# Kernel tuning notes

Hardware: AMD Instinct MI355X
Metric: run time of the kernel (lower is better)

## Reference

```python
import jax, jax.numpy as jnp
import numpy as np

DIM = 512
HEADS = 8
DIM_HEAD = 64
SLICE = 32
INNER = HEADS * DIM_HEAD  # 512


def setup_inputs() -> dict:
    key = jax.random.key(0)
    ks = jax.random.split(key, 8)
    B, N = 8, 8192
    s = 0.02
    return {
        "x": jax.random.normal(ks[0], (B, N, DIM), dtype=jnp.float32),
        "W_in": jax.random.normal(ks[1], (DIM, INNER), dtype=jnp.float32) * s,
        "b_in": jnp.zeros((INNER,), dtype=jnp.float32),
        "Wq": jax.random.normal(ks[2], (DIM_HEAD, SLICE), dtype=jnp.float32) * s,
        "Wk": jax.random.normal(ks[3], (DIM_HEAD, SLICE), dtype=jnp.float32) * s,
        "Wv": jax.random.normal(ks[4], (DIM_HEAD, DIM_HEAD), dtype=jnp.float32) * s,
        "W_out": jax.random.normal(ks[5], (INNER, DIM), dtype=jnp.float32) * s,
        "b_out": jnp.zeros((DIM,), dtype=jnp.float32),
    }


def reference(x, W_in, b_in, Wq, Wk, Wv, W_out, b_out):
    B, N, C = x.shape
    # input projection -> [B, H, N, Dh]
    x_mid = (x @ W_in + b_in).reshape(B, N, HEADS, DIM_HEAD).transpose(0, 2, 1, 3)
    q = x_mid @ Wq            # [B,H,N,S]
    k = x_mid @ Wk            # [B,H,N,S]
    v = x_mid @ Wv            # [B,H,N,Dh]
    q = jax.nn.softmax(q, axis=-1)   # over slice dim
    k = jax.nn.softmax(k, axis=-2)   # over sequence dim
    kv = jnp.einsum('bhns,bhnc->bhsc', k, v)   # [B,H,S,Dh]
    qkv = jnp.einsum('bhns,bhsc->bhnc', q, kv)  # [B,H,N,Dh]
    qkv = qkv.transpose(0, 2, 1, 3).reshape(B, N, INNER)  # b n (h d)
    return qkv @ W_out + b_out
```

## Files before the change

### kernel.cpp

```cpp
#include <hip/hip_runtime.h>
#include <cstdint>
#include <cstddef>

typedef __bf16 bf16_t;
typedef __bf16 bf16x8 __attribute__((ext_vector_type(8)));
typedef __bf16 bf16x4 __attribute__((ext_vector_type(4)));
typedef float  f32x4  __attribute__((ext_vector_type(4)));

#define HEADS    8
#define DIM_HEAD 64
#define SLICE    32
#define DIMC     512
#define NCOL     1024
#define BATCH    8
#define NSEQ     8192
#define NTOK     65536

__device__ __forceinline__ void gl2lds16(const bf16_t* g, bf16_t* l) {
  __builtin_amdgcn_global_load_lds(
      (const __attribute__((address_space(1))) uint32_t*)g,
      (__attribute__((address_space(3))) uint32_t*)l, 16, 0, 0);
}

__global__ __launch_bounds__(256) void xcast_kernel(const float* __restrict__ x,
                                                    bf16_t* __restrict__ xb) {
  const size_t i = ((size_t)blockIdx.x * 256 + threadIdx.x) * 8;
  const float4 a = *reinterpret_cast<const float4*>(x + i);
  const float4 b = *reinterpret_cast<const float4*>(x + i + 4);
  bf16x8 w;
  w[0] = (bf16_t)a.x; w[1] = (bf16_t)a.y; w[2] = (bf16_t)a.z; w[3] = (bf16_t)a.w;
  w[4] = (bf16_t)b.x; w[5] = (bf16_t)b.y; w[6] = (bf16_t)b.z; w[7] = (bf16_t)b.w;
  *reinterpret_cast<bf16x8*>(xb + i) = w;
}

__global__ __launch_bounds__(256) void wprep_kernel(
    const float* __restrict__ W_in, const float* __restrict__ b_in,
    const float* __restrict__ Wq,   const float* __restrict__ Wk,
    const float* __restrict__ Wv,
    bf16_t* __restrict__ WcT, float* __restrict__ bias_c) {
  __shared__ float sW[8192];
  for (int t = threadIdx.x; t < 2048; t += 256) { sW[t] = Wq[t]; sW[2048 + t] = Wk[t]; }
  for (int t = threadIdx.x; t < 4096; t += 256) sW[4096 + t] = Wv[t];
  __syncthreads();

  const int T  = blockIdx.x * 256 + threadIdx.x;
  const int NT = gridDim.x * 256;
  for (int idx = T; idx < NCOL * DIMC; idx += NT) {
    const int col = idx >> 9, cin = idx & 511;
    const int h = col >> 7, r = col & 127;
    int base, ldw, j;
    if (r < 32)      { j = r;      base = 0;    ldw = 32; }
    else if (r < 64) { j = r - 32; base = 2048; ldw = 32; }
    else             { j = r - 64; base = 4096; ldw = 64; }
    const float4* vp = reinterpret_cast<const float4*>(W_in + (size_t)cin * DIMC + h * DIM_HEAD);
    float acc = 0.f;
    #pragma unroll
    for (int d4 = 0; d4 < 16; ++d4) {
      const float4 v = vp[d4];
      acc += v.x * sW[base + (4*d4+0)*ldw + j];
      acc += v.y * sW[base + (4*d4+1)*ldw + j];
      acc += v.z * sW[base + (4*d4+2)*ldw + j];
      acc += v.w * sW[base + (4*d4+3)*ldw + j];
    }
    WcT[(size_t)col * DIMC + cin] = (bf16_t)acc;
  }
  if (T < NCOL) {
    const int col = T;
    const int h = col >> 7, r = col & 127;
    int base, ldw, j;
    if (r < 32)      { j = r;      base = 0;    ldw = 32; }
    else if (r < 64) { j = r - 32; base = 2048; ldw = 32; }
    else             { j = r - 64; base = 4096; ldw = 64; }
    const float* vec = b_in + h * DIM_HEAD;
    float acc = 0.f;
    #pragma unroll 8
    for (int d = 0; d < DIM_HEAD; ++d) acc += vec[d] * sW[base + d * ldw + j];
    bias_c[col] = acc;
  }
}

template<int EPI>
__global__ __launch_bounds__(256) void gemm_kernel(
    const bf16_t* __restrict__ A, const bf16_t* __restrict__ Bt,
    void* __restrict__ Cv, const float* __restrict__ bias,
    int K, int lda, int ldc,
    size_t strideA, size_t strideB, size_t strideC,
    float* __restrict__ kvp_g, float* __restrict__ denp_g)
{
  __shared__ bf16_t As[128 * 64];
  __shared__ bf16_t Bs[128 * 64];
  const int tid = threadIdx.x;
  const int p = blockIdx.y * gridDim.x + blockIdx.x;
  int mblk, nblk;
  if (EPI == 1) { mblk = (p & 7) + ((p >> 6) << 3); nblk = (p >> 3) & 7; }
  else          { mblk = (p & 7) + ((p >> 5) << 3); nblk = (p >> 3) & 3; }
  const int m0 = mblk * 128;
  const int n0 = nblk * 128;
  const int bz = blockIdx.z;
  const int wave = tid >> 6, lane = tid & 63;
  const int cg   = lane & 15, qd = lane >> 4;
  const int wm   = (wave & 1) * 64, wn = (wave >> 1) * 64;
  const int srw    = lane >> 3;
  const int gchunk = (lane & 7) ^ srw;
  const int chb    = cg & 7;

  const bf16_t* Ab = A  + strideA * bz;
  const bf16_t* Bb = Bt + strideB * bz;

  f32x4 acc[4][4];
  #pragma unroll
  for (int i = 0; i < 4; ++i)
    #pragma unroll
    for (int j = 0; j < 4; ++j) acc[i][j] = (f32x4){0.f, 0.f, 0.f, 0.f};

  for (int k0 = 0; k0 < K; k0 += 64) {
    __syncthreads();
    #pragma unroll
    for (int i = 0; i < 4; ++i) {
      const int c = wave * 4 + i;
      const int row = c * 8 + srw;
      gl2lds16(Ab + (size_t)(m0 + row) * lda + k0 + gchunk * 8, As + c * 512 + lane * 8);
    }
    #pragma unroll
    for (int i = 0; i < 4; ++i) {
      const int c = wave * 4 + i;
      const int row = c * 8 + srw;
      gl2lds16(Bb + (size_t)(n0 + row) * K + k0 + gchunk * 8, Bs + c * 512 + lane * 8);
    }
    __syncthreads();
    #pragma unroll
    for (int ks = 0; ks < 64; ks += 32) {
      const int k4 = ks >> 3;
      bf16x8 af[4], bfr[4];
      #pragma unroll
      for (int i = 0; i < 4; ++i) {
        const int ch = (qd + k4) ^ chb;
        af[i] = *reinterpret_cast<const bf16x8*>(As + (wm + 16*i + cg) * 64 + ch * 8);
      }
      #pragma unroll
      for (int j = 0; j < 4; ++j) {
        const int ch = (qd + k4) ^ chb;
        bfr[j] = *reinterpret_cast<const bf16x8*>(Bs + (wn + 16*j + cg) * 64 + ch * 8);
      }
      #pragma unroll
      for (int i = 0; i < 4; ++i)
        #pragma unroll
        for (int j = 0; j < 4; ++j)
          acc[i][j] = __builtin_amdgcn_mfma_f32_16x16x32_bf16(af[i], bfr[j], acc[i][j], 0, 0, 0);
    }
  }

  if (EPI == 1) {
    const int h   = nblk;
    const int bat = mblk >> 6;
    const int mb  = mblk & 63;
    const int bh  = bat * HEADS + h;
    __syncthreads();
    bf16_t* ekT   = As;
    bf16_t* vT    = Bs;
    float*  den_s = (float*)(void*)(As + 4096);

    if (wave < 2) {
      {
        const float b0 = bias[n0 + cg];
        const float b1 = bias[n0 + 16 + cg];
        #pragma unroll
        for (int i = 0; i < 4; ++i) {
          #pragma unroll
          for (int rr = 0; rr < 4; ++rr) {
            float v0 = acc[i][0][rr] + b0;
            float v1 = acc[i][1][rr] + b1;
            float mx = fmaxf(v0, v1);
            #pragma unroll
            for (int d = 1; d < 16; d <<= 1) mx = fmaxf(mx, __shfl_xor(mx, d, 64));
            const float e0 = __expf(v0 - mx), e1 = __expf(v1 - mx);
            float ssum = e0 + e1;
            #pragma unroll
            for (int d = 1; d < 16; d <<= 1) ssum += __shfl_xor(ssum, d, 64);
            const float rs = 1.f / ssum;
            const int row = m0 + wm + 16 * i + qd * 4 + rr;
            bf16_t* crow = (bf16_t*)Cv + (size_t)row * ldc + h * SLICE;
            crow[cg]      = (bf16_t)(e0 * rs);
            crow[16 + cg] = (bf16_t)(e1 * rs);
          }
        }
      }
      #pragma unroll
      for (int j = 2; j < 4; ++j) {
        const int s = 16 * (j - 2) + cg;
        const float bb = bias[n0 + 16 * j + cg];
        float dsum = 0.f;
        #pragma unroll
        for (int i = 0; i < 4; ++i) {
          #pragma unroll
          for (int rr = 0; rr < 4; ++rr) {
            const float e = __expf(acc[i][j][rr] + bb);
            dsum += e;
            const int n = wm + 16 * i + qd * 4 + rr;
            *(bf16_t*)((char*)ekT + (((s << 8) + 2 * n) ^ ((s & 7) << 4))) = (bf16_t)e;
          }
        }
        dsum += __shfl_xor(dsum, 16, 64);
        dsum += __shfl_xor(dsum, 32, 64);
        if (qd == 0) den_s[wave * 32 + s] = dsum;
      }
    } else {
      #pragma unroll
      for (int j = 0; j < 4; ++j) {
        const int c = 16 * j + cg;
        const float bb = bias[n0 + 64 + c];
        #pragma unroll
        for (int i = 0; i < 4; ++i) {
          #pragma unroll
          for (int rr = 0; rr < 4; ++rr) {
            const float vv = acc[i][j][rr] + bb;
            const int n = wm + 16 * i + qd * 4 + rr;
            *(bf16_t*)((char*)vT + (((c << 8) + 2 * n) ^ ((c & 7) << 4))) = (bf16_t)vv;
          }
        }
      }
    }
    __syncthreads();
    if (tid < SLICE)
      denp_g[((size_t)bh * 64 + mb) * SLICE + tid] = den_s[tid] + den_s[32 + tid];

    const int st = wave & 1;
    const int sA = st * 16 + cg;
    float* kvp = kvp_g + ((size_t)bh * 64 + mb) * (SLICE * DIM_HEAD);
    #pragma unroll
    for (int ci = 0; ci < 2; ++ci) {
      const int ct = (wave >> 1) * 2 + ci;
      const int cB = ct * 16 + cg;
      f32x4 kacc = (f32x4){0.f, 0.f, 0.f, 0.f};
      #pragma unroll
      for (int ks = 0; ks < 4; ++ks) {
        bf16x8 afr = *(const bf16x8*)((const char*)ekT +
                       (((sA << 8) + ks * 64 + qd * 16) ^ ((sA & 7) << 4)));
        bf16x8 bfr2 = *(const bf16x8*)((const char*)vT +
                       (((cB << 8) + ks * 64 + qd * 16) ^ ((cB & 7) << 4)));
        kacc = __builtin_amdgcn_mfma_f32_16x16x32_bf16(afr, bfr2, kacc, 0, 0, 0);
      }
      #pragma unroll
      for (int r = 0; r < 4; ++r)
        kvp[(st * 16 + qd * 4 + r) * DIM_HEAD + ct * 16 + cg] = kacc[r];
    }
  } else {
    #pragma unroll
    for (int j = 0; j < 4; ++j) {
      const int col = n0 + wn + 16 * j + cg;
      const float bv = bias[col];
      #pragma unroll
      for (int i = 0; i < 4; ++i) {
        #pragma unroll
        for (int rr = 0; rr < 4; ++rr) {
          const int row = m0 + wm + 16 * i + qd * 4 + rr;
          ((float*)Cv + strideC * bz)[(size_t)row * ldc + col] = acc[i][j][rr] + bv;
        }
      }
    }
  }
}

__global__ __launch_bounds__(512) void mprep_kernel(const float* __restrict__ kv_part,
                                                    const float* __restrict__ den_part,
                                                    const float* __restrict__ W_out,
                                                    bf16_t* __restrict__ Mt) {
  const int bh = blockIdx.x, bat = bh >> 3, h = bh & 7;
  const int tid = threadIdx.x;
  __shared__ float kvn[SLICE][DIM_HEAD];
  __shared__ float dsh[SLICE];
  __shared__ float wbuf[8][DIMC];
  const float* np = kv_part + (size_t)bh * 64 * (SLICE * DIM_HEAD);
  if (tid < SLICE) {
    const float* dp = den_part + (size_t)bh * 64 * SLICE;
    float d = 0.f;
    for (int mb = 0; mb < 64; ++mb) d += dp[mb * SLICE + tid];
    dsh[tid] = d;
  }
  float a0 = 0.f, a1 = 0.f, a2 = 0.f, a3 = 0.f;
  for (int mb = 0; mb < 64; ++mb) {
    const float* qp = np + (size_t)mb * (SLICE * DIM_HEAD);
    a0 += qp[tid]; a1 += qp[tid + 512]; a2 += qp[tid + 1024]; a3 += qp[tid + 1536];
  }
  __syncthreads();
  kvn[tid >> 6][tid & 63]            = a0 / dsh[tid >> 6];
  kvn[(tid + 512) >> 6][tid & 63]    = a1 / dsh[(tid + 512) >> 6];
  kvn[(tid + 1024) >> 6][tid & 63]   = a2 / dsh[(tid + 1024) >> 6];
  kvn[(tid + 1536) >> 6][tid & 63]   = a3 / dsh[(tid + 1536) >> 6];

  float accs[SLICE];
  #pragma unroll
  for (int s = 0; s < SLICE; ++s) accs[s] = 0.f;
  for (int cb = 0; cb < DIM_HEAD; cb += 8) {
    __syncthreads();
    for (int t = tid; t < 8 * DIMC; t += 512)
      wbuf[t >> 9][t & 511] = W_out[(size_t)(h * DIM_HEAD + cb + (t >> 9)) * DIMC + (t & 511)];
    __syncthreads();
    #pragma unroll
    for (int cc = 0; cc < 8; ++cc) {
      const float wv = wbuf[cc][tid];
      #pragma unroll
      for (int s = 0; s < SLICE; ++s) accs[s] += kvn[s][cb + cc] * wv;
    }
  }
  bf16_t* dst = Mt + (size_t)bat * (DIMC * 256) + (size_t)tid * 256 + h * SLICE;
  #pragma unroll
  for (int s = 0; s < SLICE; ++s) dst[s] = (bf16_t)accs[s];
}

extern "C" void kernel_launch(void* const* d_in, const int* in_sizes, int n_in,
                              void* d_out, int out_size, void* d_ws, size_t ws_size,
                              hipStream_t stream) {
  const float* x     = (const float*)d_in[0];
  const float* W_in  = (const float*)d_in[1];
  const float* b_in  = (const float*)d_in[2];
  const float* Wq    = (const float*)d_in[3];
  const float* Wk    = (const float*)d_in[4];
  const float* Wv    = (const float*)d_in[5];
  const float* W_out = (const float*)d_in[6];
  const float* b_out = (const float*)d_in[7];

  uint8_t* ws = (uint8_t*)d_ws;
  bf16_t* qprime   = (bf16_t*)(ws);
  bf16_t* WcT      = (bf16_t*)(ws + 33554432ull);
  float*  bias_c   = (float*) (ws + 34603008ull);
  float*  kv_part  = (float*) (ws + 34607104ull);
  float*  den_part = (float*) (ws + 68161536ull);
  bf16_t* Mt       = (bf16_t*)(ws + 68685824ull);
  bf16_t* xb = (bf16_t*)d_out;

  xcast_kernel<<<dim3(NTOK * DIMC / 8 / 256), dim3(256), 0, stream>>>(x, xb);
  wprep_kernel<<<dim3(256), dim3(256), 0, stream>>>(W_in, b_in, Wq, Wk, Wv, WcT, bias_c);

  gemm_kernel<1><<<dim3(8, 512, 1), dim3(256), 0, stream>>>(
      xb, WcT, (void*)qprime, bias_c,
      512 , 512 , 256 , (size_t)0, (size_t)0, (size_t)0,
      kv_part, den_part);

  mprep_kernel<<<dim3(BATCH * HEADS), dim3(512), 0, stream>>>(kv_part, den_part, W_out, Mt);

  gemm_kernel<0><<<dim3(4, 64, BATCH), dim3(256), 0, stream>>>(
      qprime, Mt, d_out, b_out,
      256 , 256 , DIMC ,
      (size_t)NSEQ * 256, (size_t)DIMC * 256, (size_t)NSEQ * DIMC,
      nullptr, nullptr);
}
```

Before: 451.2 us.

## Use 256x256 tiles with double-buffered LDS pipeline and split kv reduction

Result: slower. 502.6 us (+11.4%).

```diff
diff --git a/kernel.cpp b/kernel.cpp
--- a/kernel.cpp
+++ b/kernel.cpp
@@ -4,14 +4,12 @@
 
 typedef __bf16 bf16_t;
 typedef __bf16 bf16x8 __attribute__((ext_vector_type(8)));
-typedef __bf16 bf16x4 __attribute__((ext_vector_type(4)));
 typedef float  f32x4  __attribute__((ext_vector_type(4)));
 
 #define HEADS    8
 #define DIM_HEAD 64
 #define SLICE    32
 #define DIMC     512
-#define NCOL     1024
 #define BATCH    8
 #define NSEQ     8192
 #define NTOK     65536
@@ -45,7 +43,7 @@
 
   const int T  = blockIdx.x * 256 + threadIdx.x;
   const int NT = gridDim.x * 256;
-  for (int idx = T; idx < NCOL * DIMC; idx += NT) {
+  for (int idx = T; idx < 1024 * DIMC; idx += NT) {
     const int col = idx >> 9, cin = idx & 511;
     const int h = col >> 7, r = col & 127;
     int base, ldw, j;
@@ -64,7 +62,7 @@
     }
     WcT[(size_t)col * DIMC + cin] = (bf16_t)acc;
   }
-  if (T < NCOL) {
+  if (T < 1024) {
     const int col = T;
     const int h = col >> 7, r = col & 127;
     int base, ldw, j;
@@ -80,169 +78,180 @@
 }
 
 template<int EPI>
-__global__ __launch_bounds__(256) void gemm_kernel(
+__global__ __launch_bounds__(512, 2) void gemm_kernel(
     const bf16_t* __restrict__ A, const bf16_t* __restrict__ Bt,
     void* __restrict__ Cv, const float* __restrict__ bias,
     int K, int lda, int ldc,
     size_t strideA, size_t strideB, size_t strideC,
     float* __restrict__ kvp_g, float* __restrict__ denp_g)
 {
-  __shared__ bf16_t As[128 * 64];
-  __shared__ bf16_t Bs[128 * 64];
+  __shared__ char smem[65536];
   const int tid = threadIdx.x;
   const int p = blockIdx.y * gridDim.x + blockIdx.x;
   int mblk, nblk;
-  if (EPI == 1) { mblk = (p & 7) + ((p >> 6) << 3); nblk = (p >> 3) & 7; }
-  else          { mblk = (p & 7) + ((p >> 5) << 3); nblk = (p >> 3) & 3; }
-  const int m0 = mblk * 128;
-  const int n0 = nblk * 128;
+  if (EPI == 1) { mblk = (p & 7) + ((p >> 5) << 3); nblk = (p >> 3) & 3; }
+  else          { mblk = (p & 7) + ((p >> 4) << 3); nblk = (p >> 3) & 1; }
+  const int m0 = mblk * 256, n0 = nblk * 256;
   const int bz = blockIdx.z;
   const int wave = tid >> 6, lane = tid & 63;
-  const int cg   = lane & 15, qd = lane >> 4;
-  const int wm   = (wave & 1) * 64, wn = (wave >> 1) * 64;
-  const int srw    = lane >> 3;
-  const int gchunk = (lane & 7) ^ srw;
-  const int chb    = cg & 7;
+  const int cg = lane & 15, qd = lane >> 4;
+  const int wmi = wave >> 2;
+  const int wm = wmi * 128, wn = (wave & 3) * 64;
+  const int srow   = tid >> 2;
+  const int gchunk = (tid & 3) ^ ((tid >> 4) & 3);
 
   const bf16_t* Ab = A  + strideA * bz;
   const bf16_t* Bb = Bt + strideB * bz;
 
-  f32x4 acc[4][4];
+  auto stageA = [&](int ko, int buf) {
+    #pragma unroll
+    for (int p2 = 0; p2 < 2; ++p2)
+      gl2lds16(Ab + (size_t)(m0 + p2 * 128 + srow) * lda + ko + gchunk * 8,
+               (bf16_t*)(smem + buf * 16384 + p2 * 8192 + tid * 16));
+  };
+  auto stageB = [&](int ko, int buf) {
+    #pragma unroll
+    for (int p2 = 0; p2 < 2; ++p2)
+      gl2lds16(Bb + (size_t)(n0 + p2 * 128 + srow) * K + ko + gchunk * 8,
+               (bf16_t*)(smem + 32768 + buf * 16384 + p2 * 8192 + tid * 16));
+  };
+  auto ldA = [&](int buf, int r) -> bf16x8 {
+    return *(const bf16x8*)(smem + buf * 16384 + r * 64 + ((qd ^ ((r >> 2) & 3)) << 4));
+  };
+  auto ldB = [&](int buf, int r) -> bf16x8 {
+    return *(const bf16x8*)(smem + 32768 + buf * 16384 + r * 64 + ((qd ^ ((r >> 2) & 3)) << 4));
+  };
+
+  f32x4 acc[8][4];
   #pragma unroll
-  for (int i = 0; i < 4; ++i)
+  for (int i = 0; i < 8; ++i)
     #pragma unroll
     for (int j = 0; j < 4; ++j) acc[i][j] = (f32x4){0.f, 0.f, 0.f, 0.f};
 
-  for (int k0 = 0; k0 < K; k0 += 64) {
+  stageA(0, 0);
+  stageB(0, 0);
+
+  const int T = K >> 5;
+  int cur = 0;
+  for (int t = 0; t < T; ++t) {
+    const int nxt = cur ^ 1;
+    const int kn = (t + 1) << 5;
+    const bool pf = (t + 1 < T);
+
+    if (pf) { stageA(kn, nxt); asm volatile("s_waitcnt vmcnt(2)" ::: "memory"); }
+    else    { asm volatile("s_waitcnt vmcnt(0)" ::: "memory"); }
+    __builtin_amdgcn_s_barrier();
+
+    bf16x8 bF[4], aF[4];
+    #pragma unroll
+    for (int j = 0; j < 4; ++j) bF[j] = ldB(cur, wn + 16 * j + cg);
+    #pragma unroll
+    for (int i = 0; i < 4; ++i) aF[i] = ldA(cur, wm + 16 * i + cg);
+    __builtin_amdgcn_s_setprio(1);
+    #pragma unroll
+    for (int i = 0; i < 4; ++i)
+      #pragma unroll
+      for (int j = 0; j < 4; ++j)
+        acc[i][j] = __builtin_amdgcn_mfma_f32_16x16x32_bf16(aF[i], bF[j], acc[i][j], 0, 0, 0);
+    __builtin_amdgcn_s_setprio(0);
+
+    if (pf) stageB(kn, nxt);
+    bf16x8 aG[4];
+    #pragma unroll
+    for (int i = 0; i < 4; ++i) aG[i] = ldA(cur, wm + 64 + 16 * i + cg);
+    __builtin_amdgcn_s_setprio(1);
+    #pragma unroll
+    for (int i = 0; i < 4; ++i)
+      #pragma unroll
+      for (int j = 0; j < 4; ++j)
+        acc[i + 4][j] = __builtin_amdgcn_mfma_f32_16x16x32_bf16(aG[i], bF[j], acc[i + 4][j], 0, 0, 0);
+    __builtin_amdgcn_s_setprio(0);
+    __builtin_amdgcn_s_barrier();
+    cur = nxt;
+  }
+
+  if (EPI == 1) {
     __syncthreads();
-    #pragma unroll
-    for (int i = 0; i < 4; ++i) {
-      const int c = wave * 4 + i;
-      const int row = c * 8 + srw;
-      gl2lds16(Ab + (size_t)(m0 + row) * lda + k0 + gchunk * 8, As + c * 512 + lane * 8);
-    }
-    #pragma unroll
-    for (int i = 0; i < 4; ++i) {
-      const int c = wave * 4 + i;
-      const int row = c * 8 + srw;
-      gl2lds16(Bb + (size_t)(n0 + row) * K + k0 + gchunk * 8, Bs + c * 512 + lane * 8);
-    }
-    __syncthreads();
-    #pragma unroll
-    for (int ks = 0; ks < 64; ks += 32) {
-      const int k4 = ks >> 3;
-      bf16x8 af[4], bfr[4];
-      #pragma unroll
-      for (int i = 0; i < 4; ++i) {
-        const int ch = (qd + k4) ^ chb;
-        af[i] = *reinterpret_cast<const bf16x8*>(As + (wm + 16*i + cg) * 64 + ch * 8);
-      }
-      #pragma unroll
-      for (int j = 0; j < 4; ++j) {
-        const int ch = (qd + k4) ^ chb;
-        bfr[j] = *reinterpret_cast<const bf16x8*>(Bs + (wn + 16*j + cg) * 64 + ch * 8);
-      }
-      #pragma unroll
-      for (int i = 0; i < 4; ++i)
+    const int role = wave & 3;
+    const int bat = mblk >> 5, mb = mblk & 31;
+    char*  ekT   = smem;
+    char*  vT    = smem + 32768;
+    float* den_s = (float*)(smem + 16384);
+
+    for (int h = 0; h < 2; ++h) {
+      if (role == 2 * h) {
+        const float bq0 = bias[n0 + h * 128 + cg];
+        const float bq1 = bias[n0 + h * 128 + 16 + cg];
         #pragma unroll
-        for (int j = 0; j < 4; ++j)
-          acc[i][j] = __builtin_amdgcn_mfma_f32_16x16x32_bf16(af[i], bfr[j], acc[i][j], 0, 0, 0);
-    }
-  }
-
-  if (EPI == 1) {
-    const int h   = nblk;
-    const int bat = mblk >> 6;
-    const int mb  = mblk & 63;
-    const int bh  = bat * HEADS + h;
-    __syncthreads();
-    bf16_t* ekT   = As;
-    bf16_t* vT    = Bs;
-    float*  den_s = (float*)(void*)(As + 4096);
-
-    if (wave < 2) {
-      {
-        const float b0 = bias[n0 + cg];
-        const float b1 = bias[n0 + 16 + cg];
-        #pragma unroll
-        for (int i = 0; i < 4; ++i) {
+        for (int i = 0; i < 8; ++i) {
           #pragma unroll
           for (int rr = 0; rr < 4; ++rr) {
-            float v0 = acc[i][0][rr] + b0;
-            float v1 = acc[i][1][rr] + b1;
-            float mx = fmaxf(v0, v1);
+            const float e0 = __expf(acc[i][0][rr] + bq0);
+            const float e1 = __expf(acc[i][1][rr] + bq1);
+            float s = e0 + e1;
             #pragma unroll
-            for (int d = 1; d < 16; d <<= 1) mx = fmaxf(mx, __shfl_xor(mx, d, 64));
-            const float e0 = __expf(v0 - mx), e1 = __expf(v1 - mx);
-            float ssum = e0 + e1;
-            #pragma unroll
-            for (int d = 1; d < 16; d <<= 1) ssum += __shfl_xor(ssum, d, 64);
-            const float rs = 1.f / ssum;
+            for (int d = 1; d < 16; d <<= 1) s += __shfl_xor(s, d, 64);
+            const float rs = 1.f / s;
             const int row = m0 + wm + 16 * i + qd * 4 + rr;
-            bf16_t* crow = (bf16_t*)Cv + (size_t)row * ldc + h * SLICE;
+            bf16_t* crow = (bf16_t*)Cv + (size_t)row * ldc + (nblk * 2 + h) * SLICE;
             crow[cg]      = (bf16_t)(e0 * rs);
             crow[16 + cg] = (bf16_t)(e1 * rs);
           }
         }
-      }
-      #pragma unroll
-      for (int j = 2; j < 4; ++j) {
-        const int s = 16 * (j - 2) + cg;
-        const float bb = bias[n0 + 16 * j + cg];
-        float dsum = 0.f;
         #pragma unroll
-        for (int i = 0; i < 4; ++i) {
+        for (int j = 2; j < 4; ++j) {
+          const int s_i = 16 * (j - 2) + cg;
+          const float bk = bias[n0 + h * 128 + 32 + 16 * (j - 2) + cg];
+          float dsum = 0.f;
           #pragma unroll
-          for (int rr = 0; rr < 4; ++rr) {
-            const float e = __expf(acc[i][j][rr] + bb);
-            dsum += e;
-            const int n = wm + 16 * i + qd * 4 + rr;
-            *(bf16_t*)((char*)ekT + (((s << 8) + 2 * n) ^ ((s & 7) << 4))) = (bf16_t)e;
+          for (int i = 0; i < 8; ++i) {
+            #pragma unroll
+            for (int rr = 0; rr < 4; ++rr) {
+              const float e = __expf(acc[i][j][rr] + bk);
+              dsum += e;
+              const int n = wm + 16 * i + qd * 4 + rr;
+              *(bf16_t*)(ekT + (s_i << 9) + ((2 * n) ^ ((s_i & 7) << 4))) = (bf16_t)e;
+            }
           }
+          dsum += __shfl_xor(dsum, 16, 64);
+          dsum += __shfl_xor(dsum, 32, 64);
+          if (qd == 0) den_s[wmi * 32 + s_i] = dsum;
         }
-        dsum += __shfl_xor(dsum, 16, 64);
-        dsum += __shfl_xor(dsum, 32, 64);
-        if (qd == 0) den_s[wave * 32 + s] = dsum;
-      }
-    } else {
-      #pragma unroll
-      for (int j = 0; j < 4; ++j) {
-        const int c = 16 * j + cg;
-        const float bb = bias[n0 + 64 + c];
+      } else if (role == 2 * h + 1) {
         #pragma unroll
-        for (int i = 0; i < 4; ++i) {
+        for (int j = 0; j < 4; ++j) {
+          const int c = 16 * j + cg;
+          const float bv = bias[n0 + h * 128 + 64 + c];
           #pragma unroll
-          for (int rr = 0; rr < 4; ++rr) {
-            const float vv = acc[i][j][rr] + bb;
-            const int n = wm + 16 * i + qd * 4 + rr;
-            *(bf16_t*)((char*)vT + (((c << 8) + 2 * n) ^ ((c & 7) << 4))) = (bf16_t)vv;
+          for (int i = 0; i < 8; ++i) {
+            #pragma unroll
+            for (int rr = 0; rr < 4; ++rr) {
+              const float vv = acc[i][j][rr] + bv;
+              const int n = wm + 16 * i + qd * 4 + rr;
+              *(bf16_t*)(vT + (c << 9) + ((2 * n) ^ ((c & 7) << 4))) = (bf16_t)vv;
+            }
           }
         }
       }
-    }
-    __syncthreads();
-    if (tid < SLICE)
-      denp_g[((size_t)bh * 64 + mb) * SLICE + tid] = den_s[tid] + den_s[32 + tid];
-
-    const int st = wave & 1;
-    const int sA = st * 16 + cg;
-    float* kvp = kvp_g + ((size_t)bh * 64 + mb) * (SLICE * DIM_HEAD);
-    #pragma unroll
-    for (int ci = 0; ci < 2; ++ci) {
-      const int ct = (wave >> 1) * 2 + ci;
+      __syncthreads();
+      const int bh = bat * HEADS + nblk * 2 + h;
+      if (tid < SLICE)
+        denp_g[((size_t)bh * 32 + mb) * SLICE + tid] = den_s[tid] + den_s[32 + tid];
+      const int st = wave & 1, ct = wave >> 1;
+      const int sA = st * 16 + cg;
       const int cB = ct * 16 + cg;
       f32x4 kacc = (f32x4){0.f, 0.f, 0.f, 0.f};
       #pragma unroll
-      for (int ks = 0; ks < 4; ++ks) {
-        bf16x8 afr = *(const bf16x8*)((const char*)ekT +
-                       (((sA << 8) + ks * 64 + qd * 16) ^ ((sA & 7) << 4)));
-        bf16x8 bfr2 = *(const bf16x8*)((const char*)vT +
-                       (((cB << 8) + ks * 64 + qd * 16) ^ ((cB & 7) << 4)));
-        kacc = __builtin_amdgcn_mfma_f32_16x16x32_bf16(afr, bfr2, kacc, 0, 0, 0);
+      for (int kk = 0; kk < 8; ++kk) {
+        const bf16x8 afr = *(const bf16x8*)(ekT + (sA << 9) + ((kk * 64 + qd * 16) ^ ((sA & 7) << 4)));
+        const bf16x8 bfr = *(const bf16x8*)(vT  + (cB << 9) + ((kk * 64 + qd * 16) ^ ((cB & 7) << 4)));
+        kacc = __builtin_amdgcn_mfma_f32_16x16x32_bf16(afr, bfr, kacc, 0, 0, 0);
       }
+      float* kvp = kvp_g + ((size_t)bh * 32 + mb) * 2048;
       #pragma unroll
       for (int r = 0; r < 4; ++r)
-        kvp[(st * 16 + qd * 4 + r) * DIM_HEAD + ct * 16 + cg] = kacc[r];
+        kvp[(st * 16 + qd * 4 + r) * 64 + cB] = kacc[r];
+      __syncthreads();
     }
   } else {
     #pragma unroll
@@ -250,7 +259,7 @@
       const int col = n0 + wn + 16 * j + cg;
       const float bv = bias[col];
       #pragma unroll
-      for (int i = 0; i < 4; ++i) {
+      for (int i = 0; i < 8; ++i) {
         #pragma unroll
         for (int rr = 0; rr < 4; ++rr) {
           const int row = m0 + wm + 16 * i + qd * 4 + rr;
@@ -261,32 +270,37 @@
   }
 }
 
-__global__ __launch_bounds__(512) void mprep_kernel(const float* __restrict__ kv_part,
-                                                    const float* __restrict__ den_part,
+__global__ __launch_bounds__(256) void kvreduce_kernel(const float* __restrict__ kv_part,
+                                                       const float* __restrict__ den_part,
+                                                       float* __restrict__ kv_red,
+                                                       float* __restrict__ den_red) {
+  const int ch = blockIdx.x, bh = blockIdx.y;
+  const int tid = threadIdx.x;
+  const float* src = kv_part + (size_t)bh * 32 * 2048 + ch * 256 + tid;
+  float s = 0.f;
+  #pragma unroll
+  for (int mb = 0; mb < 32; ++mb) s += src[(size_t)mb * 2048];
+  kv_red[(size_t)bh * 2048 + ch * 256 + tid] = s;
+  if (ch == 0 && tid < 32) {
+    const float* dsrc = den_part + (size_t)bh * 32 * 32 + tid;
+    float d = 0.f;
+    #pragma unroll
+    for (int mb = 0; mb < 32; ++mb) d += dsrc[mb * 32];
+    den_red[bh * 32 + tid] = d;
+  }
+}
+
+__global__ __launch_bounds__(512) void mprep_kernel(const float* __restrict__ kv_red,
+                                                    const float* __restrict__ den_red,
                                                     const float* __restrict__ W_out,
                                                     bf16_t* __restrict__ Mt) {
   const int bh = blockIdx.x, bat = bh >> 3, h = bh & 7;
   const int tid = threadIdx.x;
   __shared__ float kvn[SLICE][DIM_HEAD];
-  __shared__ float dsh[SLICE];
   __shared__ float wbuf[8][DIMC];
-  const float* np = kv_part + (size_t)bh * 64 * (SLICE * DIM_HEAD);
-  if (tid < SLICE) {
-    const float* dp = den_part + (size_t)bh * 64 * SLICE;
-    float d = 0.f;
-    for (int mb = 0; mb < 64; ++mb) d += dp[mb * SLICE + tid];
-    dsh[tid] = d;
-  }
-  float a0 = 0.f, a1 = 0.f, a2 = 0.f, a3 = 0.f;
-  for (int mb = 0; mb < 64; ++mb) {
-    const float* qp = np + (size_t)mb * (SLICE * DIM_HEAD);
-    a0 += qp[tid]; a1 += qp[tid + 512]; a2 += qp[tid + 1024]; a3 += qp[tid + 1536];
-  }
-  __syncthreads();
-  kvn[tid >> 6][tid & 63]            = a0 / dsh[tid >> 6];
-  kvn[(tid + 512) >> 6][tid & 63]    = a1 / dsh[(tid + 512) >> 6];
-  kvn[(tid + 1024) >> 6][tid & 63]   = a2 / dsh[(tid + 1024) >> 6];
-  kvn[(tid + 1536) >> 6][tid & 63]   = a3 / dsh[(tid + 1536) >> 6];
+  const float* src = kv_red + (size_t)bh * 2048;
+  const float* dp  = den_red + bh * 32;
+  for (int t = tid; t < 2048; t += 512) kvn[t >> 6][t & 63] = src[t] / dp[t >> 6];
 
   float accs[SLICE];
   #pragma unroll
@@ -325,21 +339,24 @@
   bf16_t* WcT      = (bf16_t*)(ws + 33554432ull);
   float*  bias_c   = (float*) (ws + 34603008ull);
   float*  kv_part  = (float*) (ws + 34607104ull);
-  float*  den_part = (float*) (ws + 68161536ull);
-  bf16_t* Mt       = (bf16_t*)(ws + 68685824ull);
+  float*  den_part = (float*) (ws + 51384320ull);
+  float*  kv_red   = (float*) (ws + 51646464ull);
+  float*  den_red  = (float*) (ws + 52170752ull);
+  bf16_t* Mt       = (bf16_t*)(ws + 52178944ull);
   bf16_t* xb = (bf16_t*)d_out;
 
   xcast_kernel<<<dim3(NTOK * DIMC / 8 / 256), dim3(256), 0, stream>>>(x, xb);
   wprep_kernel<<<dim3(256), dim3(256), 0, stream>>>(W_in, b_in, Wq, Wk, Wv, WcT, bias_c);
 
-  gemm_kernel<1><<<dim3(8, 512, 1), dim3(256), 0, stream>>>(
+  gemm_kernel<1><<<dim3(8, 128, 1), dim3(512), 0, stream>>>(
       xb, WcT, (void*)qprime, bias_c,
       512 , 512 , 256 , (size_t)0, (size_t)0, (size_t)0,
       kv_part, den_part);
 
-  mprep_kernel<<<dim3(BATCH * HEADS), dim3(512), 0, stream>>>(kv_part, den_part, W_out, Mt);
-
-  gemm_kernel<0><<<dim3(4, 64, BATCH), dim3(256), 0, stream>>>(
+  kvreduce_kernel<<<dim3(8, 64), dim3(256), 0, stream>>>(kv_part, den_part, kv_red, den_red);
+  mprep_kernel<<<dim3(BATCH * HEADS), dim3(512), 0, stream>>>(kv_red, den_red, W_out, Mt);
+
+  gemm_kernel<0><<<dim3(8, 8, BATCH), dim3(512), 0, stream>>>(
       qprime, Mt, d_out, b_out,
       256 , 256 , DIMC ,
       (size_t)NSEQ * 256, (size_t)DIMC * 256, (size_t)NSEQ * DIMC,
```

## Fuse fp32-to-bf16 cast into first GEMM and parallelize kv reduction

Applied to the files above, without the earlier changes.

Result: slower. 525.4 us (+16.4%).

```diff
diff --git a/kernel.cpp b/kernel.cpp
--- a/kernel.cpp
+++ b/kernel.cpp
@@ -4,14 +4,12 @@
 
 typedef __bf16 bf16_t;
 typedef __bf16 bf16x8 __attribute__((ext_vector_type(8)));
-typedef __bf16 bf16x4 __attribute__((ext_vector_type(4)));
 typedef float  f32x4  __attribute__((ext_vector_type(4)));
 
 #define HEADS    8
 #define DIM_HEAD 64
 #define SLICE    32
 #define DIMC     512
-#define NCOL     1024
 #define BATCH    8
 #define NSEQ     8192
 #define NTOK     65536
@@ -20,17 +18,6 @@
   __builtin_amdgcn_global_load_lds(
       (const __attribute__((address_space(1))) uint32_t*)g,
       (__attribute__((address_space(3))) uint32_t*)l, 16, 0, 0);
-}
-
-__global__ __launch_bounds__(256) void xcast_kernel(const float* __restrict__ x,
-                                                    bf16_t* __restrict__ xb) {
-  const size_t i = ((size_t)blockIdx.x * 256 + threadIdx.x) * 8;
-  const float4 a = *reinterpret_cast<const float4*>(x + i);
-  const float4 b = *reinterpret_cast<const float4*>(x + i + 4);
-  bf16x8 w;
-  w[0] = (bf16_t)a.x; w[1] = (bf16_t)a.y; w[2] = (bf16_t)a.z; w[3] = (bf16_t)a.w;
-  w[4] = (bf16_t)b.x; w[5] = (bf16_t)b.y; w[6] = (bf16_t)b.z; w[7] = (bf16_t)b.w;
-  *reinterpret_cast<bf16x8*>(xb + i) = w;
 }
 
 __global__ __launch_bounds__(256) void wprep_kernel(
@@ -45,7 +32,7 @@
 
   const int T  = blockIdx.x * 256 + threadIdx.x;
   const int NT = gridDim.x * 256;
-  for (int idx = T; idx < NCOL * DIMC; idx += NT) {
+  for (int idx = T; idx < 1024 * DIMC; idx += NT) {
     const int col = idx >> 9, cin = idx & 511;
     const int h = col >> 7, r = col & 127;
     int base, ldw, j;
@@ -64,7 +51,7 @@
     }
     WcT[(size_t)col * DIMC + cin] = (bf16_t)acc;
   }
-  if (T < NCOL) {
+  if (T < 1024) {
     const int col = T;
     const int h = col >> 7, r = col & 127;
     int base, ldw, j;
@@ -79,33 +66,28 @@
   }
 }
 
-template<int EPI>
-__global__ __launch_bounds__(256) void gemm_kernel(
-    const bf16_t* __restrict__ A, const bf16_t* __restrict__ Bt,
-    void* __restrict__ Cv, const float* __restrict__ bias,
-    int K, int lda, int ldc,
-    size_t strideA, size_t strideB, size_t strideC,
+__global__ __launch_bounds__(256) void gemm1_kernel(
+    const float* __restrict__ X, const bf16_t* __restrict__ Bt,
+    bf16_t* __restrict__ qprime, const float* __restrict__ bias,
     float* __restrict__ kvp_g, float* __restrict__ denp_g)
 {
   __shared__ bf16_t As[128 * 64];
   __shared__ bf16_t Bs[128 * 64];
   const int tid = threadIdx.x;
   const int p = blockIdx.y * gridDim.x + blockIdx.x;
-  int mblk, nblk;
-  if (EPI == 1) { mblk = (p & 7) + ((p >> 6) << 3); nblk = (p >> 3) & 7; }
-  else          { mblk = (p & 7) + ((p >> 5) << 3); nblk = (p >> 3) & 3; }
-  const int m0 = mblk * 128;
-  const int n0 = nblk * 128;
-  const int bz = blockIdx.z;
+  const int mblk = (p & 7) + ((p >> 6) << 3);
+  const int nblk = (p >> 3) & 7;
+  const int m0 = mblk * 128, n0 = nblk * 128;
   const int wave = tid >> 6, lane = tid & 63;
-  const int cg   = lane & 15, qd = lane >> 4;
-  const int wm   = (wave & 1) * 64, wn = (wave >> 1) * 64;
-  const int srw    = lane >> 3;
+  const int cg = lane & 15, qd = lane >> 4;
+  const int wm = (wave & 1) * 64, wn = (wave >> 1) * 64;
+  const int srw = lane >> 3;
   const int gchunk = (lane & 7) ^ srw;
-  const int chb    = cg & 7;
-
-  const bf16_t* Ab = A  + strideA * bz;
-  const bf16_t* Bb = Bt + strideB * bz;
+  const int chb = cg & 7;
+
+  const int arow = tid >> 1;
+  const int akh  = (tid & 1) * 32;
+  const float* xrow = X + (size_t)(m0 + arow) * DIMC + akh;
 
   f32x4 acc[4][4];
   #pragma unroll
@@ -113,21 +95,39 @@
     #pragma unroll
     for (int j = 0; j < 4; ++j) acc[i][j] = (f32x4){0.f, 0.f, 0.f, 0.f};
 
-  for (int k0 = 0; k0 < K; k0 += 64) {
+  float4 xr[8];
+  #pragma unroll
+  for (int l = 0; l < 8; ++l) xr[l] = *reinterpret_cast<const float4*>(xrow + l * 4);
+
+  for (int k0 = 0; k0 < DIMC; k0 += 64) {
     __syncthreads();
+    #pragma unroll
+    for (int c = 0; c < 4; ++c) {
+      const float4 u = xr[2 * c], v = xr[2 * c + 1];
+      bf16x8 w;
+      w[0] = (bf16_t)u.x; w[1] = (bf16_t)u.y; w[2] = (bf16_t)u.z; w[3] = (bf16_t)u.w;
+      w[4] = (bf16_t)v.x; w[5] = (bf16_t)v.y; w[6] = (bf16_t)v.z; w[7] = (bf16_t)v.w;
+      const int g = (akh >> 3) + c;
+      *reinterpret_cast<bf16x8*>(As + arow * 64 + ((g ^ (arow & 7)) << 3)) = w;
+    }
     #pragma unroll
     for (int i = 0; i < 4; ++i) {
       const int c = wave * 4 + i;
       const int row = c * 8 + srw;
-      gl2lds16(Ab + (size_t)(m0 + row) * lda + k0 + gchunk * 8, As + c * 512 + lane * 8);
-    }
-    #pragma unroll
-    for (int i = 0; i < 4; ++i) {
-      const int c = wave * 4 + i;
-      const int row = c * 8 + srw;
-      gl2lds16(Bb + (size_t)(n0 + row) * K + k0 + gchunk * 8, Bs + c * 512 + lane * 8);
-    }
-    __syncthreads();
+      gl2lds16(Bt + (size_t)(n0 + row) * DIMC + k0 + gchunk * 8, Bs + c * 512 + lane * 8);
+    }
+    __builtin_amdgcn_sched_barrier(0);
+    if (k0 + 64 < DIMC) {
+      #pragma unroll
+      for (int l = 0; l < 8; ++l)
+        xr[l] = *reinterpret_cast<const float4*>(xrow + k0 + 64 + l * 4);
+      asm volatile("s_waitcnt vmcnt(8)" ::: "memory");
+    } else {
+      asm volatile("s_waitcnt vmcnt(0)" ::: "memory");
+    }
+    asm volatile("s_waitcnt lgkmcnt(0)" ::: "memory");
+    __builtin_amdgcn_sched_barrier(0);
+    __builtin_amdgcn_s_barrier();
     #pragma unroll
     for (int ks = 0; ks < 64; ks += 32) {
       const int k4 = ks >> 3;
@@ -135,12 +135,12 @@
       #pragma unroll
       for (int i = 0; i < 4; ++i) {
         const int ch = (qd + k4) ^ chb;
-        af[i] = *reinterpret_cast<const bf16x8*>(As + (wm + 16*i + cg) * 64 + ch * 8);
+        af[i] = *reinterpret_cast<const bf16x8*>(As + (wm + 16 * i + cg) * 64 + ch * 8);
       }
       #pragma unroll
       for (int j = 0; j < 4; ++j) {
         const int ch = (qd + k4) ^ chb;
-        bfr[j] = *reinterpret_cast<const bf16x8*>(Bs + (wn + 16*j + cg) * 64 + ch * 8);
+        bfr[j] = *reinterpret_cast<const bf16x8*>(Bs + (wn + 16 * j + cg) * 64 + ch * 8);
       }
       #pragma unroll
       for (int i = 0; i < 4; ++i)
@@ -150,151 +150,222 @@
     }
   }
 
-  if (EPI == 1) {
-    const int h   = nblk;
-    const int bat = mblk >> 6;
-    const int mb  = mblk & 63;
-    const int bh  = bat * HEADS + h;
-    __syncthreads();
-    bf16_t* ekT   = As;
-    bf16_t* vT    = Bs;
-    float*  den_s = (float*)(void*)(As + 4096);
-
-    if (wave < 2) {
-      {
-        const float b0 = bias[n0 + cg];
-        const float b1 = bias[n0 + 16 + cg];
-        #pragma unroll
-        for (int i = 0; i < 4; ++i) {
-          #pragma unroll
-          for (int rr = 0; rr < 4; ++rr) {
-            float v0 = acc[i][0][rr] + b0;
-            float v1 = acc[i][1][rr] + b1;
-            float mx = fmaxf(v0, v1);
-            #pragma unroll
-            for (int d = 1; d < 16; d <<= 1) mx = fmaxf(mx, __shfl_xor(mx, d, 64));
-            const float e0 = __expf(v0 - mx), e1 = __expf(v1 - mx);
-            float ssum = e0 + e1;
-            #pragma unroll
-            for (int d = 1; d < 16; d <<= 1) ssum += __shfl_xor(ssum, d, 64);
-            const float rs = 1.f / ssum;
-            const int row = m0 + wm + 16 * i + qd * 4 + rr;
-            bf16_t* crow = (bf16_t*)Cv + (size_t)row * ldc + h * SLICE;
-            crow[cg]      = (bf16_t)(e0 * rs);
-            crow[16 + cg] = (bf16_t)(e1 * rs);
-          }
-        }
-      }
-      #pragma unroll
-      for (int j = 2; j < 4; ++j) {
-        const int s = 16 * (j - 2) + cg;
-        const float bb = bias[n0 + 16 * j + cg];
-        float dsum = 0.f;
-        #pragma unroll
-        for (int i = 0; i < 4; ++i) {
-          #pragma unroll
-          for (int rr = 0; rr < 4; ++rr) {
-            const float e = __expf(acc[i][j][rr] + bb);
-            dsum += e;
-            const int n = wm + 16 * i + qd * 4 + rr;
-            *(bf16_t*)((char*)ekT + (((s << 8) + 2 * n) ^ ((s & 7) << 4))) = (bf16_t)e;
-          }
-        }
-        dsum += __shfl_xor(dsum, 16, 64);
-        dsum += __shfl_xor(dsum, 32, 64);
-        if (qd == 0) den_s[wave * 32 + s] = dsum;
-      }
-    } else {
-      #pragma unroll
-      for (int j = 0; j < 4; ++j) {
-        const int c = 16 * j + cg;
-        const float bb = bias[n0 + 64 + c];
-        #pragma unroll
-        for (int i = 0; i < 4; ++i) {
-          #pragma unroll
-          for (int rr = 0; rr < 4; ++rr) {
-            const float vv = acc[i][j][rr] + bb;
-            const int n = wm + 16 * i + qd * 4 + rr;
-            *(bf16_t*)((char*)vT + (((c << 8) + 2 * n) ^ ((c & 7) << 4))) = (bf16_t)vv;
-          }
-        }
-      }
-    }
-    __syncthreads();
-    if (tid < SLICE)
-      denp_g[((size_t)bh * 64 + mb) * SLICE + tid] = den_s[tid] + den_s[32 + tid];
-
-    const int st = wave & 1;
-    const int sA = st * 16 + cg;
-    float* kvp = kvp_g + ((size_t)bh * 64 + mb) * (SLICE * DIM_HEAD);
-    #pragma unroll
-    for (int ci = 0; ci < 2; ++ci) {
-      const int ct = (wave >> 1) * 2 + ci;
-      const int cB = ct * 16 + cg;
-      f32x4 kacc = (f32x4){0.f, 0.f, 0.f, 0.f};
-      #pragma unroll
-      for (int ks = 0; ks < 4; ++ks) {
-        bf16x8 afr = *(const bf16x8*)((const char*)ekT +
-                       (((sA << 8) + ks * 64 + qd * 16) ^ ((sA & 7) << 4)));
-        bf16x8 bfr2 = *(const bf16x8*)((const char*)vT +
-                       (((cB << 8) + ks * 64 + qd * 16) ^ ((cB & 7) << 4)));
-        kacc = __builtin_amdgcn_mfma_f32_16x16x32_bf16(afr, bfr2, kacc, 0, 0, 0);
-      }
-      #pragma unroll
-      for (int r = 0; r < 4; ++r)
-        kvp[(st * 16 + qd * 4 + r) * DIM_HEAD + ct * 16 + cg] = kacc[r];
-    }
-  } else {
-    #pragma unroll
-    for (int j = 0; j < 4; ++j) {
-      const int col = n0 + wn + 16 * j + cg;
-      const float bv = bias[col];
+  const int h   = nblk;
+  const int bat = mblk >> 6;
+  const int mb  = mblk & 63;
+  const int bh  = bat * HEADS + h;
+  __syncthreads();
+  bf16_t* ekT   = As;
+  bf16_t* vT    = Bs;
+  float*  den_s = (float*)(void*)(As + 4096);
+
+  if (wave < 2) {
+    {
+      const float b0 = bias[n0 + cg];
+      const float b1 = bias[n0 + 16 + cg];
       #pragma unroll
       for (int i = 0; i < 4; ++i) {
         #pragma unroll
         for (int rr = 0; rr < 4; ++rr) {
+          float v0 = acc[i][0][rr] + b0;
+          float v1 = acc[i][1][rr] + b1;
+          float mx = fmaxf(v0, v1);
+          #pragma unroll
+          for (int d = 1; d < 16; d <<= 1) mx = fmaxf(mx, __shfl_xor(mx, d, 64));
+          const float e0 = __expf(v0 - mx), e1 = __expf(v1 - mx);
+          float s = e0 + e1;
+          #pragma unroll
+          for (int d = 1; d < 16; d <<= 1) s += __shfl_xor(s, d, 64);
+          const float rs = 1.f / s;
           const int row = m0 + wm + 16 * i + qd * 4 + rr;
-          ((float*)Cv + strideC * bz)[(size_t)row * ldc + col] = acc[i][j][rr] + bv;
+          bf16_t* crow = qprime + (size_t)row * 256 + h * SLICE;
+          crow[cg]      = (bf16_t)(e0 * rs);
+          crow[16 + cg] = (bf16_t)(e1 * rs);
         }
       }
     }
-  }
-}
-
-__global__ __launch_bounds__(512) void mprep_kernel(const float* __restrict__ kv_part,
-                                                    const float* __restrict__ den_part,
+    #pragma unroll
+    for (int j = 2; j < 4; ++j) {
+      const int s_i = 16 * (j - 2) + cg;
+      const float bk = bias[n0 + 16 * j + cg];
+      float dsum = 0.f;
+      #pragma unroll
+      for (int i = 0; i < 4; ++i) {
+        #pragma unroll
+        for (int rr = 0; rr < 4; ++rr) {
+          const float e = __expf(acc[i][j][rr] + bk);
+          dsum += e;
+          const int n = wm + 16 * i + qd * 4 + rr;
+          *(bf16_t*)((char*)ekT + (((s_i << 8) + 2 * n) ^ ((s_i & 7) << 4))) = (bf16_t)e;
+        }
+      }
+      dsum += __shfl_xor(dsum, 16, 64);
+      dsum += __shfl_xor(dsum, 32, 64);
+      if (qd == 0) den_s[wave * 32 + s_i] = dsum;
+    }
+  } else {
+    #pragma unroll
+    for (int j = 0; j < 4; ++j) {
+      const int c = 16 * j + cg;
+      const float bv = bias[n0 + 64 + c];
+      #pragma unroll
+      for (int i = 0; i < 4; ++i) {
+        #pragma unroll
+        for (int rr = 0; rr < 4; ++rr) {
+          const float vv = acc[i][j][rr] + bv;
+          const int n = wm + 16 * i + qd * 4 + rr;
+          *(bf16_t*)((char*)vT + (((c << 8) + 2 * n) ^ ((c & 7) << 4))) = (bf16_t)vv;
+        }
+      }
+    }
+  }
+  __syncthreads();
+  if (tid < SLICE)
+    denp_g[((size_t)bh * 64 + mb) * SLICE + tid] = den_s[tid] + den_s[32 + tid];
+
+  const int st = wave & 1;
+  const int sA = st * 16 + cg;
+  float* kvp = kvp_g + ((size_t)bh * 64 + mb) * (SLICE * DIM_HEAD);
+  #pragma unroll
+  for (int ci = 0; ci < 2; ++ci) {
+    const int ct = (wave >> 1) * 2 + ci;
+    const int cB = ct * 16 + cg;
+    f32x4 kacc = (f32x4){0.f, 0.f, 0.f, 0.f};
+    #pragma unroll
+    for (int ks = 0; ks < 4; ++ks) {
+      bf16x8 afr = *(const bf16x8*)((const char*)ekT +
+                     (((sA << 8) + ks * 64 + qd * 16) ^ ((sA & 7) << 4)));
+      bf16x8 bfr2 = *(const bf16x8*)((const char*)vT +
+                     (((cB << 8) + ks * 64 + qd * 16) ^ ((cB & 7) << 4)));
+      kacc = __builtin_amdgcn_mfma_f32_16x16x32_bf16(afr, bfr2, kacc, 0, 0, 0);
+    }
+    #pragma unroll
+    for (int r = 0; r < 4; ++r)
+      kvp[(st * 16 + qd * 4 + r) * DIM_HEAD + cB] = kacc[r];
+  }
+}
+
+__global__ __launch_bounds__(256) void gemm3_kernel(
+    const bf16_t* __restrict__ A, const bf16_t* __restrict__ Bt,
+    float* __restrict__ out, const float* __restrict__ bias)
+{
+  __shared__ bf16_t As[128 * 64];
+  __shared__ bf16_t Bs[128 * 64];
+  const int tid = threadIdx.x;
+  const int p = blockIdx.y * gridDim.x + blockIdx.x;
+  const int mblk = (p & 7) + ((p >> 5) << 3);
+  const int nblk = (p >> 3) & 3;
+  const int m0 = mblk * 128, n0 = nblk * 128;
+  const int bz = blockIdx.z;
+  const int wave = tid >> 6, lane = tid & 63;
+  const int cg = lane & 15, qd = lane >> 4;
+  const int wm = (wave & 1) * 64, wn = (wave >> 1) * 64;
+  const int srw = lane >> 3;
+  const int gchunk = (lane & 7) ^ srw;
+  const int chb = cg & 7;
+
+  const bf16_t* Ab = A + (size_t)bz * NSEQ * 256;
+  const bf16_t* Bb = Bt + (size_t)bz * DIMC * 256;
+
+  f32x4 acc[4][4];
+  #pragma unroll
+  for (int i = 0; i < 4; ++i)
+    #pragma unroll
+    for (int j = 0; j < 4; ++j) acc[i][j] = (f32x4){0.f, 0.f, 0.f, 0.f};
+
+  for (int k0 = 0; k0 < 256; k0 += 64) {
+    __syncthreads();
+    #pragma unroll
+    for (int i = 0; i < 4; ++i) {
+      const int c = wave * 4 + i;
+      const int row = c * 8 + srw;
+      gl2lds16(Ab + (size_t)(m0 + row) * 256 + k0 + gchunk * 8, As + c * 512 + lane * 8);
+    }
+    #pragma unroll
+    for (int i = 0; i < 4; ++i) {
+      const int c = wave * 4 + i;
+      const int row = c * 8 + srw;
+      gl2lds16(Bb + (size_t)(n0 + row) * 256 + k0 + gchunk * 8, Bs + c * 512 + lane * 8);
+    }
+    __syncthreads();
+    #pragma unroll
+    for (int ks = 0; ks < 64; ks += 32) {
+      const int k4 = ks >> 3;
+      bf16x8 af[4], bfr[4];
+      #pragma unroll
+      for (int i = 0; i < 4; ++i) {
+        const int ch = (qd + k4) ^ chb;
+        af[i] = *reinterpret_cast<const bf16x8*>(As + (wm + 16 * i + cg) * 64 + ch * 8);
+      }
+      #pragma unroll
+      for (int j = 0; j < 4; ++j) {
+        const int ch = (qd + k4) ^ chb;
+        bfr[j] = *reinterpret_cast<const bf16x8*>(Bs + (wn + 16 * j + cg) * 64 + ch * 8);
+      }
+      #pragma unroll
+      for (int i = 0; i < 4; ++i)
+        #pragma unroll
+        for (int j = 0; j < 4; ++j)
+          acc[i][j] = __builtin_amdgcn_mfma_f32_16x16x32_bf16(af[i], bfr[j], acc[i][j], 0, 0, 0);
+    }
+  }
+
+  float* ob = out + (size_t)bz * NSEQ * DIMC;
+  #pragma unroll
+  for (int j = 0; j < 4; ++j) {
+    const int col = n0 + wn + 16 * j + cg;
+    const float bv = bias[col];
+    #pragma unroll
+    for (int i = 0; i < 4; ++i) {
+      #pragma unroll
+      for (int rr = 0; rr < 4; ++rr) {
+        const int row = m0 + wm + 16 * i + qd * 4 + rr;
+        ob[(size_t)row * DIMC + col] = acc[i][j][rr] + bv;
+      }
+    }
+  }
+}
+
+__global__ __launch_bounds__(256) void kvreduce_kernel(const float* __restrict__ kv_part,
+                                                       const float* __restrict__ den_part,
+                                                       float* __restrict__ kv_red,
+                                                       float* __restrict__ den_red) {
+  const int ch = blockIdx.x, bh = blockIdx.y;
+  const int tid = threadIdx.x;
+  const float* src = kv_part + (size_t)bh * 64 * 2048 + ch * 256 + tid;
+  float s = 0.f;
+  #pragma unroll 8
+  for (int mb = 0; mb < 64; ++mb) s += src[(size_t)mb * 2048];
+  kv_red[(size_t)bh * 2048 + ch * 256 + tid] = s;
+  if (ch == 0 && tid < 32) {
+    const float* dsrc = den_part + (size_t)bh * 64 * 32 + tid;
+    float d = 0.f;
+    #pragma unroll 8
+    for (int mb = 0; mb < 64; ++mb) d += dsrc[mb * 32];
+    den_red[bh * 32 + tid] = d;
+  }
+}
+
+__global__ __launch_bounds__(256) void mprep_kernel(const float* __restrict__ kv_red,
+                                                    const float* __restrict__ den_red,
                                                     const float* __restrict__ W_out,
                                                     bf16_t* __restrict__ Mt) {
-  const int bh = blockIdx.x, bat = bh >> 3, h = bh & 7;
+  const int bh = blockIdx.x, half = blockIdx.y;
+  const int bat = bh >> 3, h = bh & 7;
   const int tid = threadIdx.x;
   __shared__ float kvn[SLICE][DIM_HEAD];
-  __shared__ float dsh[SLICE];
-  __shared__ float wbuf[8][DIMC];
-  const float* np = kv_part + (size_t)bh * 64 * (SLICE * DIM_HEAD);
-  if (tid < SLICE) {
-    const float* dp = den_part + (size_t)bh * 64 * SLICE;
-    float d = 0.f;
-    for (int mb = 0; mb < 64; ++mb) d += dp[mb * SLICE + tid];
-    dsh[tid] = d;
-  }
-  float a0 = 0.f, a1 = 0.f, a2 = 0.f, a3 = 0.f;
-  for (int mb = 0; mb < 64; ++mb) {
-    const float* qp = np + (size_t)mb * (SLICE * DIM_HEAD);
-    a0 += qp[tid]; a1 += qp[tid + 512]; a2 += qp[tid + 1024]; a3 += qp[tid + 1536];
-  }
-  __syncthreads();
-  kvn[tid >> 6][tid & 63]            = a0 / dsh[tid >> 6];
-  kvn[(tid + 512) >> 6][tid & 63]    = a1 / dsh[(tid + 512) >> 6];
-  kvn[(tid + 1024) >> 6][tid & 63]   = a2 / dsh[(tid + 1024) >> 6];
-  kvn[(tid + 1536) >> 6][tid & 63]   = a3 / dsh[(tid + 1536) >> 6];
+  __shared__ float wbuf[8][256];
+  const float* src = kv_red + (size_t)bh * 2048;
+  const float* dp  = den_red + bh * 32;
+  for (int t = tid; t < 2048; t += 256) kvn[t >> 6][t & 63] = src[t] / dp[t >> 6];
 
   float accs[SLICE];
   #pragma unroll
   for (int s = 0; s < SLICE; ++s) accs[s] = 0.f;
   for (int cb = 0; cb < DIM_HEAD; cb += 8) {
     __syncthreads();
-    for (int t = tid; t < 8 * DIMC; t += 512)
-      wbuf[t >> 9][t & 511] = W_out[(size_t)(h * DIM_HEAD + cb + (t >> 9)) * DIMC + (t & 511)];
+    for (int t = tid; t < 8 * 256; t += 256)
+      wbuf[t >> 8][t & 255] = W_out[(size_t)(h * DIM_HEAD + cb + (t >> 8)) * DIMC + half * 256 + (t & 255)];
     __syncthreads();
     #pragma unroll
     for (int cc = 0; cc < 8; ++cc) {
@@ -303,7 +374,7 @@
       for (int s = 0; s < SLICE; ++s) accs[s] += kvn[s][cb + cc] * wv;
     }
   }
-  bf16_t* dst = Mt + (size_t)bat * (DIMC * 256) + (size_t)tid * 256 + h * SLICE;
+  bf16_t* dst = Mt + (size_t)bat * (DIMC * 256) + (size_t)(half * 256 + tid) * 256 + h * SLICE;
   #pragma unroll
   for (int s = 0; s < SLICE; ++s) dst[s] = (bf16_t)accs[s];
 }
@@ -326,22 +397,18 @@
   float*  bias_c   = (float*) (ws + 34603008ull);
   float*  kv_part  = (float*) (ws + 34607104ull);
   float*  den_part = (float*) (ws + 68161536ull);
-  bf16_t* Mt       = (bf16_t*)(ws + 68685824ull);
-  bf16_t* xb = (bf16_t*)d_out;
-
-  xcast_kernel<<<dim3(NTOK * DIMC / 8 / 256), dim3(256), 0, stream>>>(x, xb);
+  float*  kv_red   = (float*) (ws + 68685824ull);
+  float*  den_red  = (float*) (ws + 69210112ull);
+  bf16_t* Mt       = (bf16_t*)(ws + 69218304ull);
+
   wprep_kernel<<<dim3(256), dim3(256), 0, stream>>>(W_in, b_in, Wq, Wk, Wv, WcT, bias_c);
 
-  gemm_kernel<1><<<dim3(8, 512, 1), dim3(256), 0, stream>>>(
-      xb, WcT, (void*)qprime, bias_c,
-      512 , 512 , 256 , (size_t)0, (size_t)0, (size_t)0,
-      kv_part, den_part);
-
-  mprep_kernel<<<dim3(BATCH * HEADS), dim3(512), 0, stream>>>(kv_part, den_part, W_out, Mt);
-
-  gemm_kernel<0><<<dim3(4, 64, BATCH), dim3(256), 0, stream>>>(
-      qprime, Mt, d_out, b_out,
-      256 , 256 , DIMC ,
-      (size_t)NSEQ * 256, (size_t)DIMC * 256, (size_t)NSEQ * DIMC,
-      nullptr, nullptr);
-}
+  gemm1_kernel<<<dim3(8, 512), dim3(256), 0, stream>>>(
+      x, WcT, qprime, bias_c, kv_part, den_part);
+
+  kvreduce_kernel<<<dim3(8, 64), dim3(256), 0, stream>>>(kv_part, den_part, kv_red, den_red);
+  mprep_kernel<<<dim3(64, 2), dim3(256), 0, stream>>>(kv_red, den_red, W_out, Mt);
+
+  gemm3_kernel<<<dim3(4, 64, BATCH), dim3(256), 0, stream>>>(
+      qprime, Mt, (float*)d_out, b_out);
+}
```
